# Kernel optimization log

Measured on AMD Instinct MI355X. Metric: run time of the kernel, lower is better.

Reference implementation:

```python
import jax, jax.numpy as jnp
import numpy as np

KH, KW = 3, 3
PAD = 1
C_IN, C_OUT = 64, 128


def unfold(x, kh, kw, pad):
    # x: (B, C, H, W) -> (B, C, kh*kw, H*W), torch.nn.functional.unfold ordering
    B, C, H, W = x.shape
    xp = jnp.pad(x, ((0, 0), (0, 0), (pad, pad), (pad, pad)))
    patches = jnp.stack(
        [xp[:, :, i:i + H, j:j + W] for i in range(kh) for j in range(kw)],
        axis=2,
    )  # (B, C, K, H, W)
    return patches.reshape(B, C, kh * kw, H * W)


def setup_inputs() -> dict:
    key = jax.random.key(0)
    k1, k2, k3 = jax.random.split(key, 3)
    B, H, W = 8, 128, 128
    inp = jax.random.normal(k1, (B, C_IN, H, W), dtype=jnp.float32)
    g_buffer = jax.random.uniform(k2, (B, 2, H, W), dtype=jnp.float32)
    # weights param as in torch: (1, C*kh*kw, 1, out_channels), kaiming-uniform-ish
    wdepth = C_IN * KH * KW
    bound = float(np.sqrt(6.0 / wdepth))
    weights = jax.random.uniform(k3, (1, wdepth, 1, C_OUT), dtype=jnp.float32,
                                 minval=-bound, maxval=bound)
    bias = jnp.zeros((C_OUT,), dtype=jnp.float32)
    return {"input": inp, "g_buffer": g_buffer, "weights": weights, "bias": bias}


def reference(input, g_buffer, weights, bias):
    B, C, H, W = input.shape
    K = KH * KW
    L = H * W
    depth = 2.0 * (g_buffer[:, -1:, :, :] - 0.5)  # (B, 1, H, W)

    input_unf = unfold(input, KH, KW, PAD)          # (B, C, K, L)
    depth_unf = unfold(depth, KH, KW, PAD)          # (B, 1, K, L)

    # bilateral depth weighting
    dfeat = depth_unf - depth.reshape(B, 1, 1, L)   # (B, 1, K, L)
    dfeat = jnp.sum(dfeat * dfeat, axis=1)          # (B, K, L)
    wf = jnp.exp(-dfeat)
    wf = 9.0 * wf / jnp.sum(wf, axis=1, keepdims=True)  # (B, K, L)

    filt = input_unf * wf[:, None, :, :]            # (B, C, K, L)
    filt = filt.reshape(B, C * K, L)

    W2 = weights.reshape(C_OUT, C * K)              # raw reshape, matches torch .view
    out_unf = jnp.einsum('bkl,ok->bol', filt, W2)   # (B, C_OUT, L)
    out = out_unf.reshape(B, C_OUT, H, W) + bias[None, :, None, None]
    return out
```

## Files before the change

kernel.cpp:

```cpp
#include <hip/hip_runtime.h>
#include <hip/hip_bf16.h>
#include <stdint.h>

typedef _Float16 f16x8 __attribute__((ext_vector_type(8)));
typedef float    f32x4 __attribute__((ext_vector_type(4)));

#define CIN   64
#define COUT  128
#define HH    128
#define WW    128
#define BB    8

#define TROW  130
#define ROWBYTES (130 * 128)
#define TSIZE ((size_t)BB * TROW * ROWBYTES)

#define LROWB (34 * 128)
#define NCHKT (4 * 272)

#define AS1 __attribute__((address_space(1)))
#define AS3 __attribute__((address_space(3)))


__global__ void prep_plus(const float* __restrict__ wflat, _Float16* __restrict__ bp,
                          _Float16* __restrict__ T) {
    int gid = blockIdx.x * 256 + threadIdx.x;
    if (gid < 8 * 18 * 64 * 8) {
        int j = gid & 7;
        int l = (gid >> 3) & 63;
        int s = (gid >> 9) % 18;
        int n = gid / (18 * 512);
        int o = n * 16 + (l & 15);
        int c = ((s & 1) << 5) + ((l >> 4) << 3) + j;
        int k = s >> 1;
        bp[gid] = (_Float16)wflat[o * 576 + c * 9 + k];
        return;
    }
    int h = gid - 8 * 18 * 64 * 8;
    if (h < 16 * 1040) {
        int row = h / 1040, c = h - row * 1040;
        int b = row >> 1, yp = (row & 1) * 129;
        f16x8 z = {};
        *(f16x8*)((char*)T + (size_t)(b * TROW + yp) * ROWBYTES + c * 16) = z;
    }
}

__global__ __launch_bounds__(256) void transpose_pass(const float* __restrict__ inp,
                                                      _Float16* __restrict__ T) {
    __shared__ float sT[64][129];
    const int b   = blockIdx.x >> 7;
    const int y   = blockIdx.x & 127;
    const int tid = threadIdx.x;

    const float* ib = inp + ((long)b * CIN * HH + y) * WW;
    const int xq = tid & 31, c8 = tid >> 5;
    #pragma unroll
    for (int i = 0; i < 8; ++i) {
        int c = c8 * 8 + i;
        float4 v = *(const float4*)(ib + (long)c * (HH * WW) + (xq << 2));
        *(float4*)&sT[c][xq << 2] = v;
    }
    __syncthreads();

    const int x  = tid & 127;
    const int ch = tid >> 7;
    char* rowp = (char*)T + (size_t)(b * TROW + y + 1) * ROWBYTES + (size_t)(x + 1) * 128;
    const int sw = (x + 1) & 7;
    for (int c0 = ch * 8; c0 < 64; c0 += 16) {
        f16x8 v;
        #pragma unroll
        for (int j = 0; j < 8; ++j) v[j] = (_Float16)sT[c0 + j][x];
        *(f16x8*)(rowp + (((c0 >> 3) ^ sw) << 4)) = v;
    }
    if (tid < 16) {
        char* basep = (char*)T + (size_t)(b * TROW + y + 1) * ROWBYTES
                    + ((tid >> 3) ? 129 * 128 : 0) + (tid & 7) * 16;
        f16x8 z = {};
        *(f16x8*)basep = z;
    }
}

__global__ __launch_bounds__(256, 4) void depthcnn_main(
    const _Float16* __restrict__ T, const float* __restrict__ gbuf,
    const float* __restrict__ bias, const _Float16* __restrict__ aprep,
    float* __restrict__ out)
{
    __shared__ __align__(1024) char sIn[4 * LROWB];
    __shared__ _Float16 sWf[2][9][36];

    const int blk    = blockIdx.x;
    const int b      = blk & 7;
    const int rest   = blk >> 3;
    const int strip  = rest & 63;
    const int xq     = rest >> 6;
    const int ystart = strip << 1;
    const int x0     = xq << 5;

    const int tid  = threadIdx.x;
    const int wave = tid >> 6;
    const int lane = tid & 63;
    const int oi   = wave;
    const int l15  = lane & 15;
    const int g4   = lane >> 4;

    {
        const char* Tb = (const char*)T + ((size_t)b * TROW + ystart) * ROWBYTES
                       + (size_t)x0 * 128;
        #pragma unroll
        for (int tt = 0; tt < 5; ++tt) {
            int t = tt * 256 + tid;
            if (t < NCHKT) {
                int tr = t / 272, c = t - tr * 272;
                __builtin_amdgcn_global_load_lds(
                    (const AS1 uint32_t*)(Tb + (size_t)tr * ROWBYTES + c * 16),
                    (AS3 uint32_t*)(sIn + tr * LROWB + c * 16), 16, 0, 0);
            }
        }
    }

    const f16x8* __restrict__ ap = (const f16x8*)aprep;
    const char* wp0 = (const char*)ap + (size_t)((oi * 2 + 0) * 18) * 1024 + lane * 16;
    const char* wp1 = (const char*)ap + (size_t)((oi * 2 + 1) * 18) * 1024 + lane * 16;
    f16x8 af[2][2][2];
    af[0][0][0] = *(const f16x8*)(wp0);
    af[0][0][1] = *(const f16x8*)(wp0 + 1024);
    af[0][1][0] = *(const f16x8*)(wp1);
    af[0][1][1] = *(const f16x8*)(wp1 + 1024);

    if (tid < 64) {
        const int r = tid >> 5, pxl = tid & 31, x = x0 + pxl, y = ystart + r;
        const float* g = gbuf + ((size_t)b * 2 + 1) * (HH * WW);
        float dc = 2.f * (g[y * WW + x] - 0.5f);
        float e[9];
        float ssum = 0.f;
        #pragma unroll
        for (int k = 0; k < 9; ++k) {
            int yy = y + (k / 3) - 1;
            int xx = x + (k % 3) - 1;
            float dn = 0.f;
            if ((unsigned)yy < 128u && (unsigned)xx < 128u)
                dn = 2.f * (g[yy * WW + xx] - 0.5f);
            float df = dn - dc;
            float ek = __expf(-df * df);
            e[k] = ek;
            ssum += ek;
        }
        float sc = 9.f / ssum;
        #pragma unroll
        for (int k = 0; k < 9; ++k) sWf[r][k][pxl] = (_Float16)(e[k] * sc);
    }

    __syncthreads();

    const char* binA[3][2];
    #pragma unroll
    for (int d = 0; d < 3; ++d)
        #pragma unroll
        for (int ch = 0; ch < 2; ++ch)
            binA[d][ch] = sIn + (((l15 + d) << 7)
                        + ((((ch << 2) | g4) ^ ((l15 + d) & 7)) << 4));
    const char* bwf = (const char*)&sWf[0][0][0] + l15 * 2;

    f32x4 acc[2][2][2];
    #pragma unroll
    for (int r = 0; r < 2; ++r)
        #pragma unroll
        for (int t2 = 0; t2 < 2; ++t2)
            #pragma unroll
            for (int pt = 0; pt < 2; ++pt)
                acc[r][t2][pt] = (f32x4){0.f, 0.f, 0.f, 0.f};

    #pragma unroll
    for (int k = 0; k < 9; ++k) {
        if (k < 8) {
            const char* q0 = wp0 + (k + 1) * 2048;
            const char* q1 = wp1 + (k + 1) * 2048;
            af[(k + 1) & 1][0][0] = *(const f16x8*)(q0);
            af[(k + 1) & 1][0][1] = *(const f16x8*)(q0 + 1024);
            af[(k + 1) & 1][1][0] = *(const f16x8*)(q1);
            af[(k + 1) & 1][1][1] = *(const f16x8*)(q1 + 1024);
        }
        const int dy = k / 3;
        const int dx = k - 3 * dy;
        #pragma unroll
        for (int r = 0; r < 2; ++r) {
            _Float16 wh[2];
            #pragma unroll
            for (int pt = 0; pt < 2; ++pt)
                wh[pt] = *(const _Float16*)(bwf + ((r * 9 + k) * 72 + pt * 32));
            #pragma unroll
            for (int ch = 0; ch < 2; ++ch) {
                f16x8 bf[2];
                #pragma unroll
                for (int pt = 0; pt < 2; ++pt) {
                    f16x8 iv = *(const f16x8*)(binA[dx][ch]
                             + ((r + dy) * LROWB + (pt << 11)));
                    f16x8 w8 = {wh[pt], wh[pt], wh[pt], wh[pt],
                                wh[pt], wh[pt], wh[pt], wh[pt]};
                    bf[pt] = iv * w8;
                }
                #pragma unroll
                for (int t2 = 0; t2 < 2; ++t2)
                    #pragma unroll
                    for (int pt = 0; pt < 2; ++pt)
                        acc[r][t2][pt] = __builtin_amdgcn_mfma_f32_16x16x32_f16(
                            af[k & 1][t2][ch], bf[pt], acc[r][t2][pt], 0, 0, 0);
            }
        }
    }

    float* ob = out + (size_t)b * COUT * (HH * WW) + x0;
    #pragma unroll
    for (int r = 0; r < 2; ++r) {
        const int y = ystart + r;
        #pragma unroll
        for (int t2 = 0; t2 < 2; ++t2) {
            #pragma unroll
            for (int pt = 0; pt < 2; ++pt) {
                #pragma unroll
                for (int r4 = 0; r4 < 4; ++r4) {
                    const int o = (oi << 5) + (t2 << 4) + (g4 << 2) + r4;
                    ob[(size_t)o * (HH * WW) + (size_t)y * WW + (pt << 4) + l15]
                        = acc[r][t2][pt][r4] + bias[o];
                }
            }
        }
    }
}

extern "C" void kernel_launch(void* const* d_in, const int* in_sizes, int n_in,
                              void* d_out, int out_size, void* d_ws, size_t ws_size,
                              hipStream_t stream) {
    const float* inp  = (const float*)d_in[0];
    const float* gbuf = (const float*)d_in[1];
    const float* wts  = (const float*)d_in[2];
    const float* bias = (const float*)d_in[3];

    _Float16* T  = (_Float16*)d_ws;
    _Float16* bp = (_Float16*)((char*)d_ws + TSIZE);

    hipLaunchKernelGGL(prep_plus, dim3(353), dim3(256), 0, stream, wts, bp, T);
    hipLaunchKernelGGL(transpose_pass, dim3(BB * HH), dim3(256), 0, stream, inp, T);
    hipLaunchKernelGGL(depthcnn_main, dim3(2048), dim3(256), 0, stream,
                       T, gbuf, bias, bp, (float*)d_out);
}
```

Baseline: 49.60 us.

## Process four rows per block with overlapped second-strip halo load

Each block now handles four output rows as two 2-row strips instead of one strip, halving the grid to 1024 blocks. The extra two halo rows and their depth weights are loaded while the first strip's MFMA work runs, so the input halo rows are reused across strips and the load latency is hidden. This trades lower grid parallelism and more LDS per block for less redundant halo traffic and fewer block launches. Weight fragments are reloaded per strip.

```diff
diff --git a/kernel.cpp b/kernel.cpp
--- a/kernel.cpp
+++ b/kernel.cpp
@@ -16,7 +16,6 @@
 #define TSIZE ((size_t)BB * TROW * ROWBYTES)
 
 #define LROWB (34 * 128)
-#define NCHKT (4 * 272)
 
 #define AS1 __attribute__((address_space(1)))
 #define AS3 __attribute__((address_space(3)))
@@ -85,15 +84,15 @@
     const float* __restrict__ bias, const _Float16* __restrict__ aprep,
     float* __restrict__ out)
 {
-    __shared__ __align__(1024) char sIn[4 * LROWB];
-    __shared__ _Float16 sWf[2][9][36];
+    __shared__ __align__(1024) char sIn[6 * LROWB];
+    __shared__ _Float16 sWf[4][9][36];
 
     const int blk    = blockIdx.x;
     const int b      = blk & 7;
     const int rest   = blk >> 3;
-    const int strip  = rest & 63;
-    const int xq     = rest >> 6;
-    const int ystart = strip << 1;
+    const int grp    = rest & 31;
+    const int xq     = rest >> 5;
+    const int ystart = grp << 2;
     const int x0     = xq << 5;
 
     const int tid  = threadIdx.x;
@@ -103,33 +102,28 @@
     const int l15  = lane & 15;
     const int g4   = lane >> 4;
 
-    {
-        const char* Tb = (const char*)T + ((size_t)b * TROW + ystart) * ROWBYTES
-                       + (size_t)x0 * 128;
-        #pragma unroll
-        for (int tt = 0; tt < 5; ++tt) {
-            int t = tt * 256 + tid;
-            if (t < NCHKT) {
-                int tr = t / 272, c = t - tr * 272;
-                __builtin_amdgcn_global_load_lds(
-                    (const AS1 uint32_t*)(Tb + (size_t)tr * ROWBYTES + c * 16),
-                    (AS3 uint32_t*)(sIn + tr * LROWB + c * 16), 16, 0, 0);
-            }
+    const char* Tb = (const char*)T + ((size_t)b * TROW + ystart) * ROWBYTES
+                   + (size_t)x0 * 128;
+    const float* g = gbuf + ((size_t)b * 2 + 1) * (HH * WW);
+
+    #pragma unroll
+    for (int tt = 0; tt < 5; ++tt) {
+        int t = tt * 256 + tid;
+        if (t < 1088) {
+            int tr = t / 272, c = t - tr * 272;
+            __builtin_amdgcn_global_load_lds(
+                (const AS1 uint32_t*)(Tb + (size_t)tr * ROWBYTES + c * 16),
+                (AS3 uint32_t*)(sIn + tr * LROWB + c * 16), 16, 0, 0);
         }
     }
 
     const f16x8* __restrict__ ap = (const f16x8*)aprep;
     const char* wp0 = (const char*)ap + (size_t)((oi * 2 + 0) * 18) * 1024 + lane * 16;
     const char* wp1 = (const char*)ap + (size_t)((oi * 2 + 1) * 18) * 1024 + lane * 16;
-    f16x8 af[2][2][2];
-    af[0][0][0] = *(const f16x8*)(wp0);
-    af[0][0][1] = *(const f16x8*)(wp0 + 1024);
-    af[0][1][0] = *(const f16x8*)(wp1);
-    af[0][1][1] = *(const f16x8*)(wp1 + 1024);
-
-    if (tid < 64) {
-        const int r = tid >> 5, pxl = tid & 31, x = x0 + pxl, y = ystart + r;
-        const float* g = gbuf + ((size_t)b * 2 + 1) * (HH * WW);
+
+    if ((tid & 3) == 0) {
+        const int idx = tid >> 2;
+        const int r = idx >> 5, pxl = idx & 31, x = x0 + pxl, y = ystart + r;
         float dc = 2.f * (g[y * WW + x] - 0.5f);
         float e[9];
         float ssum = 0.f;
@@ -152,6 +146,39 @@
 
     __syncthreads();
 
+    #pragma unroll
+    for (int tt = 0; tt < 3; ++tt) {
+        int t = tt * 256 + tid;
+        if (t < 544) {
+            int tr = t / 272, c = t - tr * 272;
+            __builtin_amdgcn_global_load_lds(
+                (const AS1 uint32_t*)(Tb + (size_t)(4 + tr) * ROWBYTES + c * 16),
+                (AS3 uint32_t*)(sIn + (4 + tr) * LROWB + c * 16), 16, 0, 0);
+        }
+    }
+    if ((tid & 3) == 0) {
+        const int idx = tid >> 2;
+        const int r = 2 + (idx >> 5), pxl = idx & 31, x = x0 + pxl, y = ystart + r;
+        float dc = 2.f * (g[y * WW + x] - 0.5f);
+        float e[9];
+        float ssum = 0.f;
+        #pragma unroll
+        for (int k = 0; k < 9; ++k) {
+            int yy = y + (k / 3) - 1;
+            int xx = x + (k % 3) - 1;
+            float dn = 0.f;
+            if ((unsigned)yy < 128u && (unsigned)xx < 128u)
+                dn = 2.f * (g[yy * WW + xx] - 0.5f);
+            float df = dn - dc;
+            float ek = __expf(-df * df);
+            e[k] = ek;
+            ssum += ek;
+        }
+        float sc = 9.f / ssum;
+        #pragma unroll
+        for (int k = 0; k < 9; ++k) sWf[r][k][pxl] = (_Float16)(e[k] * sc);
+    }
+
     const char* binA[3][2];
     #pragma unroll
     for (int d = 0; d < 3; ++d)
@@ -161,71 +188,86 @@
                         + ((((ch << 2) | g4) ^ ((l15 + d) & 7)) << 4));
     const char* bwf = (const char*)&sWf[0][0][0] + l15 * 2;
 
-    f32x4 acc[2][2][2];
-    #pragma unroll
-    for (int r = 0; r < 2; ++r)
-        #pragma unroll
-        for (int t2 = 0; t2 < 2; ++t2)
-            #pragma unroll
-            for (int pt = 0; pt < 2; ++pt)
-                acc[r][t2][pt] = (f32x4){0.f, 0.f, 0.f, 0.f};
-
-    #pragma unroll
-    for (int k = 0; k < 9; ++k) {
-        if (k < 8) {
-            const char* q0 = wp0 + (k + 1) * 2048;
-            const char* q1 = wp1 + (k + 1) * 2048;
-            af[(k + 1) & 1][0][0] = *(const f16x8*)(q0);
-            af[(k + 1) & 1][0][1] = *(const f16x8*)(q0 + 1024);
-            af[(k + 1) & 1][1][0] = *(const f16x8*)(q1);
-            af[(k + 1) & 1][1][1] = *(const f16x8*)(q1 + 1024);
-        }
-        const int dy = k / 3;
-        const int dx = k - 3 * dy;
-        #pragma unroll
-        for (int r = 0; r < 2; ++r) {
-            _Float16 wh[2];
-            #pragma unroll
-            for (int pt = 0; pt < 2; ++pt)
-                wh[pt] = *(const _Float16*)(bwf + ((r * 9 + k) * 72 + pt * 32));
-            #pragma unroll
-            for (int ch = 0; ch < 2; ++ch) {
-                f16x8 bf[2];
-                #pragma unroll
-                for (int pt = 0; pt < 2; ++pt) {
-                    f16x8 iv = *(const f16x8*)(binA[dx][ch]
-                             + ((r + dy) * LROWB + (pt << 11)));
-                    f16x8 w8 = {wh[pt], wh[pt], wh[pt], wh[pt],
-                                wh[pt], wh[pt], wh[pt], wh[pt]};
-                    bf[pt] = iv * w8;
-                }
-                #pragma unroll
-                for (int t2 = 0; t2 < 2; ++t2)
-                    #pragma unroll
-                    for (int pt = 0; pt < 2; ++pt)
-                        acc[r][t2][pt] = __builtin_amdgcn_mfma_f32_16x16x32_f16(
-                            af[k & 1][t2][ch], bf[pt], acc[r][t2][pt], 0, 0, 0);
-            }
-        }
-    }
-
     float* ob = out + (size_t)b * COUT * (HH * WW) + x0;
-    #pragma unroll
-    for (int r = 0; r < 2; ++r) {
-        const int y = ystart + r;
-        #pragma unroll
-        for (int t2 = 0; t2 < 2; ++t2) {
-            #pragma unroll
-            for (int pt = 0; pt < 2; ++pt) {
-                #pragma unroll
-                for (int r4 = 0; r4 < 4; ++r4) {
-                    const int o = (oi << 5) + (t2 << 4) + (g4 << 2) + r4;
-                    ob[(size_t)o * (HH * WW) + (size_t)y * WW + (pt << 4) + l15]
-                        = acc[r][t2][pt][r4] + bias[o];
-                }
-            }
-        }
-    }
+
+#define KSTRIP(S)                                                                  \
+    {                                                                              \
+        f32x4 acc[2][2][2];                                                        \
+        _Pragma("unroll")                                                          \
+        for (int r = 0; r < 2; ++r)                                                \
+            _Pragma("unroll")                                                      \
+            for (int t2 = 0; t2 < 2; ++t2)                                         \
+                _Pragma("unroll")                                                  \
+                for (int pt = 0; pt < 2; ++pt)                                     \
+                    acc[r][t2][pt] = (f32x4){0.f, 0.f, 0.f, 0.f};                  \
+        f16x8 af[2][2][2];                                                         \
+        af[0][0][0] = *(const f16x8*)(wp0);                                        \
+        af[0][0][1] = *(const f16x8*)(wp0 + 1024);                                 \
+        af[0][1][0] = *(const f16x8*)(wp1);                                        \
+        af[0][1][1] = *(const f16x8*)(wp1 + 1024);                                 \
+        _Pragma("unroll")                                                          \
+        for (int k = 0; k < 9; ++k) {                                              \
+            if (k < 8) {                                                           \
+                const char* q0 = wp0 + (k + 1) * 2048;                             \
+                const char* q1 = wp1 + (k + 1) * 2048;                             \
+                af[(k + 1) & 1][0][0] = *(const f16x8*)(q0);                       \
+                af[(k + 1) & 1][0][1] = *(const f16x8*)(q0 + 1024);                \
+                af[(k + 1) & 1][1][0] = *(const f16x8*)(q1);                       \
+                af[(k + 1) & 1][1][1] = *(const f16x8*)(q1 + 1024);                \
+            }                                                                      \
+            const int dy = k / 3;                                                  \
+            const int dx = k - 3 * dy;                                             \
+            _Pragma("unroll")                                                      \
+            for (int r = 0; r < 2; ++r) {                                          \
+                _Float16 wh[2];                                                    \
+                _Pragma("unroll")                                                  \
+                for (int pt = 0; pt < 2; ++pt)                                     \
+                    wh[pt] = *(const _Float16*)(bwf                                \
+                           + (((2 * (S) + r) * 9 + k) * 72 + pt * 32));            \
+                _Pragma("unroll")                                                  \
+                for (int ch = 0; ch < 2; ++ch) {                                   \
+                    f16x8 bf[2];                                                   \
+                    _Pragma("unroll")                                              \
+                    for (int pt = 0; pt < 2; ++pt) {                               \
+                        f16x8 iv = *(const f16x8*)(binA[dx][ch]                    \
+                                 + ((2 * (S) + r + dy) * LROWB + (pt << 11)));     \
+                        f16x8 w8 = {wh[pt], wh[pt], wh[pt], wh[pt],                \
+                                    wh[pt], wh[pt], wh[pt], wh[pt]};               \
+                        bf[pt] = iv * w8;                                          \
+                    }                                                              \
+                    _Pragma("unroll")                                              \
+                    for (int t2 = 0; t2 < 2; ++t2)                                 \
+                        _Pragma("unroll")                                          \
+                        for (int pt = 0; pt < 2; ++pt)                             \
+                            acc[r][t2][pt] = __builtin_amdgcn_mfma_f32_16x16x32_f16( \
+                                af[k & 1][t2][ch], bf[pt], acc[r][t2][pt], 0, 0, 0); \
+                }                                                                  \
+            }                                                                      \
+        }                                                                          \
+        _Pragma("unroll")                                                          \
+        for (int r = 0; r < 2; ++r) {                                              \
+            const int y = ystart + 2 * (S) + r;                                    \
+            _Pragma("unroll")                                                      \
+            for (int t2 = 0; t2 < 2; ++t2) {                                       \
+                _Pragma("unroll")                                                  \
+                for (int pt = 0; pt < 2; ++pt) {                                   \
+                    _Pragma("unroll")                                              \
+                    for (int r4 = 0; r4 < 4; ++r4) {                               \
+                        const int o = (oi << 5) + (t2 << 4) + (g4 << 2) + r4;      \
+                        ob[(size_t)o * (HH * WW) + (size_t)y * WW + (pt << 4) + l15] \
+                            = acc[r][t2][pt][r4] + bias[o];                        \
+                    }                                                              \
+                }                                                                  \
+            }                                                                      \
+        }                                                                          \
+    }
+
+    KSTRIP(0)
+
+    __syncthreads();
+
+    KSTRIP(1)
+#undef KSTRIP
 }
 
 extern "C" void kernel_launch(void* const* d_in, const int* in_sizes, int n_in,
@@ -241,6 +283,6 @@
 
     hipLaunchKernelGGL(prep_plus, dim3(353), dim3(256), 0, stream, wts, bp, T);
     hipLaunchKernelGGL(transpose_pass, dim3(BB * HH), dim3(256), 0, stream, inp, T);
-    hipLaunchKernelGGL(depthcnn_main, dim3(2048), dim3(256), 0, stream,
+    hipLaunchKernelGGL(depthcnn_main, dim3(1024), dim3(256), 0, stream,
                        T, gbuf, bias, bp, (float*)d_out);
 }
```

New measurement: 58.11 us. 17.2% more time.

## Read activation tiles directly from global memory instead of staging in LDS

Applied to the files above, without the earlier changes.

The main kernel no longer copies the 4-row input halo tile into shared memory with global_load_lds. Each lane now loads its B-operand vectors straight from the transposed fp16 buffer, relying on L1/L2 caching for the 3x3 neighbourhood reuse. The XOR swizzle in the transpose pass is removed to match the plain addressing. This cuts LDS use (raising possible occupancy) and removes the staging step, but puts repeated, partly redundant global loads on the MFMA inner loop's critical path.

```diff
diff --git a/kernel.cpp b/kernel.cpp
--- a/kernel.cpp
+++ b/kernel.cpp
@@ -14,12 +14,6 @@
 #define TROW  130
 #define ROWBYTES (130 * 128)
 #define TSIZE ((size_t)BB * TROW * ROWBYTES)
-
-#define LROWB (34 * 128)
-#define NCHKT (4 * 272)
-
-#define AS1 __attribute__((address_space(1)))
-#define AS3 __attribute__((address_space(3)))
 
 
 __global__ void prep_plus(const float* __restrict__ wflat, _Float16* __restrict__ bp,
@@ -65,12 +59,11 @@
     const int x  = tid & 127;
     const int ch = tid >> 7;
     char* rowp = (char*)T + (size_t)(b * TROW + y + 1) * ROWBYTES + (size_t)(x + 1) * 128;
-    const int sw = (x + 1) & 7;
     for (int c0 = ch * 8; c0 < 64; c0 += 16) {
         f16x8 v;
         #pragma unroll
         for (int j = 0; j < 8; ++j) v[j] = (_Float16)sT[c0 + j][x];
-        *(f16x8*)(rowp + (((c0 >> 3) ^ sw) << 4)) = v;
+        *(f16x8*)(rowp + c0 * 2) = v;
     }
     if (tid < 16) {
         char* basep = (char*)T + (size_t)(b * TROW + y + 1) * ROWBYTES
@@ -85,7 +78,6 @@
     const float* __restrict__ bias, const _Float16* __restrict__ aprep,
     float* __restrict__ out)
 {
-    __shared__ __align__(1024) char sIn[4 * LROWB];
     __shared__ _Float16 sWf[2][9][36];
 
     const int blk    = blockIdx.x;
@@ -103,20 +95,11 @@
     const int l15  = lane & 15;
     const int g4   = lane >> 4;
 
-    {
-        const char* Tb = (const char*)T + ((size_t)b * TROW + ystart) * ROWBYTES
-                       + (size_t)x0 * 128;
-        #pragma unroll
-        for (int tt = 0; tt < 5; ++tt) {
-            int t = tt * 256 + tid;
-            if (t < NCHKT) {
-                int tr = t / 272, c = t - tr * 272;
-                __builtin_amdgcn_global_load_lds(
-                    (const AS1 uint32_t*)(Tb + (size_t)tr * ROWBYTES + c * 16),
-                    (AS3 uint32_t*)(sIn + tr * LROWB + c * 16), 16, 0, 0);
-            }
-        }
-    }
+    const char* Tb = (const char*)T + ((size_t)b * TROW + ystart) * ROWBYTES
+                   + (size_t)x0 * 128 + (l15 << 7) + (g4 << 4);
+    const char* btr[4];
+    #pragma unroll
+    for (int tr = 0; tr < 4; ++tr) btr[tr] = Tb + tr * ROWBYTES;
 
     const f16x8* __restrict__ ap = (const f16x8*)aprep;
     const char* wp0 = (const char*)ap + (size_t)((oi * 2 + 0) * 18) * 1024 + lane * 16;
@@ -152,13 +135,6 @@
 
     __syncthreads();
 
-    const char* binA[3][2];
-    #pragma unroll
-    for (int d = 0; d < 3; ++d)
-        #pragma unroll
-        for (int ch = 0; ch < 2; ++ch)
-            binA[d][ch] = sIn + (((l15 + d) << 7)
-                        + ((((ch << 2) | g4) ^ ((l15 + d) & 7)) << 4));
     const char* bwf = (const char*)&sWf[0][0][0] + l15 * 2;
 
     f32x4 acc[2][2][2];
@@ -193,8 +169,8 @@
                 f16x8 bf[2];
                 #pragma unroll
                 for (int pt = 0; pt < 2; ++pt) {
-                    f16x8 iv = *(const f16x8*)(binA[dx][ch]
-                             + ((r + dy) * LROWB + (pt << 11)));
+                    f16x8 iv = *(const f16x8*)(btr[r + dy]
+                             + ((pt << 11) + dx * 128 + ch * 64));
                     f16x8 w8 = {wh[pt], wh[pt], wh[pt], wh[pt],
                                 wh[pt], wh[pt], wh[pt], wh[pt]};
                     bf[pt] = iv * w8;
```

Result: slower. 83.30 us (+67.9%).

## Retile main kernel so each block covers full row width and all outputs

Applied to the files above, without the earlier changes.

The main conv kernel now assigns each block two full image rows (128 pixels) and has every wave compute all 128 output channels for its own 32-pixel slice, instead of splitting output channels across waves over a 32-pixel window. The block loads whole padded rows into LDS once, which removes the overlapping halo loads and the redundant depth-weight computation done by the previous four x-quarter blocks. Each wave now keeps a larger accumulator set and streams all weight fragments, and MFMA sections are wrapped in s_setprio. The trade-off is a grid that shrinks from 2048 to 512 blocks, more registers and LDS per block, and lower occupancy (launch bounds lowered to 2).

```diff
diff --git a/kernel.cpp b/kernel.cpp
--- a/kernel.cpp
+++ b/kernel.cpp
@@ -14,9 +14,6 @@
 #define TROW  130
 #define ROWBYTES (130 * 128)
 #define TSIZE ((size_t)BB * TROW * ROWBYTES)
-
-#define LROWB (34 * 128)
-#define NCHKT (4 * 272)
 
 #define AS1 __attribute__((address_space(1)))
 #define AS3 __attribute__((address_space(3)))
@@ -80,63 +77,56 @@
     }
 }
 
-__global__ __launch_bounds__(256, 4) void depthcnn_main(
+__global__ __launch_bounds__(256, 2) void depthcnn_main(
     const _Float16* __restrict__ T, const float* __restrict__ gbuf,
     const float* __restrict__ bias, const _Float16* __restrict__ aprep,
     float* __restrict__ out)
 {
-    __shared__ __align__(1024) char sIn[4 * LROWB];
-    __shared__ _Float16 sWf[2][9][36];
+    __shared__ __align__(1024) char sIn[4 * ROWBYTES];
+    __shared__ _Float16 sWf[2][9][128];
 
     const int blk    = blockIdx.x;
     const int b      = blk & 7;
-    const int rest   = blk >> 3;
-    const int strip  = rest & 63;
-    const int xq     = rest >> 6;
+    const int strip  = blk >> 3;
     const int ystart = strip << 1;
-    const int x0     = xq << 5;
 
     const int tid  = threadIdx.x;
     const int wave = tid >> 6;
     const int lane = tid & 63;
-    const int oi   = wave;
     const int l15  = lane & 15;
     const int g4   = lane >> 4;
+    const int x0w  = wave << 5;
 
     {
-        const char* Tb = (const char*)T + ((size_t)b * TROW + ystart) * ROWBYTES
-                       + (size_t)x0 * 128;
-        #pragma unroll
-        for (int tt = 0; tt < 5; ++tt) {
+        const char* Tb = (const char*)T + ((size_t)b * TROW + ystart) * ROWBYTES;
+        #pragma unroll
+        for (int tt = 0; tt < 17; ++tt) {
             int t = tt * 256 + tid;
-            if (t < NCHKT) {
-                int tr = t / 272, c = t - tr * 272;
+            if (t < 4 * 1040) {
+                int tr = t / 1040, c = t - tr * 1040;
                 __builtin_amdgcn_global_load_lds(
                     (const AS1 uint32_t*)(Tb + (size_t)tr * ROWBYTES + c * 16),
-                    (AS3 uint32_t*)(sIn + tr * LROWB + c * 16), 16, 0, 0);
-            }
-        }
-    }
-
-    const f16x8* __restrict__ ap = (const f16x8*)aprep;
-    const char* wp0 = (const char*)ap + (size_t)((oi * 2 + 0) * 18) * 1024 + lane * 16;
-    const char* wp1 = (const char*)ap + (size_t)((oi * 2 + 1) * 18) * 1024 + lane * 16;
-    f16x8 af[2][2][2];
-    af[0][0][0] = *(const f16x8*)(wp0);
-    af[0][0][1] = *(const f16x8*)(wp0 + 1024);
-    af[0][1][0] = *(const f16x8*)(wp1);
-    af[0][1][1] = *(const f16x8*)(wp1 + 1024);
-
-    if (tid < 64) {
-        const int r = tid >> 5, pxl = tid & 31, x = x0 + pxl, y = ystart + r;
+                    (AS3 uint32_t*)(sIn + tr * ROWBYTES + c * 16), 16, 0, 0);
+            }
+        }
+    }
+
+    const char* ap = (const char*)aprep + lane * 16;
+    f16x8 af[2][8];
+    #pragma unroll
+    for (int ot = 0; ot < 8; ++ot)
+        af[0][ot] = *(const f16x8*)(ap + (size_t)(ot * 18) * 1024);
+
+    {
+        const int r = tid >> 7, px = tid & 127, y = ystart + r;
         const float* g = gbuf + ((size_t)b * 2 + 1) * (HH * WW);
-        float dc = 2.f * (g[y * WW + x] - 0.5f);
+        float dc = 2.f * (g[y * WW + px] - 0.5f);
         float e[9];
         float ssum = 0.f;
         #pragma unroll
         for (int k = 0; k < 9; ++k) {
             int yy = y + (k / 3) - 1;
-            int xx = x + (k % 3) - 1;
+            int xx = px + (k % 3) - 1;
             float dn = 0.f;
             if ((unsigned)yy < 128u && (unsigned)xx < 128u)
                 dn = 2.f * (g[yy * WW + xx] - 0.5f);
@@ -147,7 +137,7 @@
         }
         float sc = 9.f / ssum;
         #pragma unroll
-        for (int k = 0; k < 9; ++k) sWf[r][k][pxl] = (_Float16)(e[k] * sc);
+        for (int k = 0; k < 9; ++k) sWf[r][k][px] = (_Float16)(e[k] * sc);
     }
 
     __syncthreads();
@@ -157,71 +147,71 @@
     for (int d = 0; d < 3; ++d)
         #pragma unroll
         for (int ch = 0; ch < 2; ++ch)
-            binA[d][ch] = sIn + (((l15 + d) << 7)
+            binA[d][ch] = sIn + (x0w << 7) + (((l15 + d) << 7)
                         + ((((ch << 2) | g4) ^ ((l15 + d) & 7)) << 4));
-    const char* bwf = (const char*)&sWf[0][0][0] + l15 * 2;
-
-    f32x4 acc[2][2][2];
+    const char* bwf = (const char*)&sWf[0][0][0] + ((x0w + l15) << 1);
+
+    f32x4 acc[2][2][8];
     #pragma unroll
     for (int r = 0; r < 2; ++r)
         #pragma unroll
-        for (int t2 = 0; t2 < 2; ++t2)
-            #pragma unroll
-            for (int pt = 0; pt < 2; ++pt)
-                acc[r][t2][pt] = (f32x4){0.f, 0.f, 0.f, 0.f};
-
-    #pragma unroll
-    for (int k = 0; k < 9; ++k) {
-        if (k < 8) {
-            const char* q0 = wp0 + (k + 1) * 2048;
-            const char* q1 = wp1 + (k + 1) * 2048;
-            af[(k + 1) & 1][0][0] = *(const f16x8*)(q0);
-            af[(k + 1) & 1][0][1] = *(const f16x8*)(q0 + 1024);
-            af[(k + 1) & 1][1][0] = *(const f16x8*)(q1);
-            af[(k + 1) & 1][1][1] = *(const f16x8*)(q1 + 1024);
-        }
-        const int dy = k / 3;
-        const int dx = k - 3 * dy;
+        for (int pt = 0; pt < 2; ++pt)
+            #pragma unroll
+            for (int ot = 0; ot < 8; ++ot)
+                acc[r][pt][ot] = (f32x4){0.f, 0.f, 0.f, 0.f};
+
+    #pragma unroll
+    for (int s = 0; s < 18; ++s) {
+        if (s < 17) {
+            #pragma unroll
+            for (int ot = 0; ot < 8; ++ot)
+                af[(s + 1) & 1][ot] = *(const f16x8*)(ap + (size_t)(ot * 18 + s + 1) * 1024);
+        }
+        const int tap = s >> 1;
+        const int ch  = s & 1;
+        const int dy  = tap / 3;
+        const int dx  = tap - 3 * dy;
         #pragma unroll
         for (int r = 0; r < 2; ++r) {
             _Float16 wh[2];
             #pragma unroll
             for (int pt = 0; pt < 2; ++pt)
-                wh[pt] = *(const _Float16*)(bwf + ((r * 9 + k) * 72 + pt * 32));
-            #pragma unroll
-            for (int ch = 0; ch < 2; ++ch) {
-                f16x8 bf[2];
+                wh[pt] = *(const _Float16*)(bwf + ((r * 9 + tap) * 256 + pt * 32));
+            f16x8 bf[2];
+            #pragma unroll
+            for (int pt = 0; pt < 2; ++pt) {
+                f16x8 iv = *(const f16x8*)(binA[dx][ch]
+                         + ((r + dy) * ROWBYTES + (pt << 11)));
+                f16x8 w8 = {wh[pt], wh[pt], wh[pt], wh[pt],
+                            wh[pt], wh[pt], wh[pt], wh[pt]};
+                bf[pt] = iv * w8;
+            }
+            __builtin_amdgcn_s_setprio(1);
+            #pragma unroll
+            for (int ot = 0; ot < 8; ++ot) {
+                acc[r][0][ot] = __builtin_amdgcn_mfma_f32_16x16x32_f16(
+                    af[s & 1][ot], bf[0], acc[r][0][ot], 0, 0, 0);
+                acc[r][1][ot] = __builtin_amdgcn_mfma_f32_16x16x32_f16(
+                    af[s & 1][ot], bf[1], acc[r][1][ot], 0, 0, 0);
+            }
+            __builtin_amdgcn_s_setprio(0);
+        }
+    }
+
+    float* ob = out + (size_t)b * COUT * (HH * WW);
+    #pragma unroll
+    for (int ot = 0; ot < 8; ++ot) {
+        #pragma unroll
+        for (int r4 = 0; r4 < 4; ++r4) {
+            const int o = (ot << 4) + (g4 << 2) + r4;
+            const float bv = bias[o];
+            #pragma unroll
+            for (int r = 0; r < 2; ++r) {
                 #pragma unroll
                 for (int pt = 0; pt < 2; ++pt) {
-                    f16x8 iv = *(const f16x8*)(binA[dx][ch]
-                             + ((r + dy) * LROWB + (pt << 11)));
-                    f16x8 w8 = {wh[pt], wh[pt], wh[pt], wh[pt],
-                                wh[pt], wh[pt], wh[pt], wh[pt]};
-                    bf[pt] = iv * w8;
-                }
-                #pragma unroll
-                for (int t2 = 0; t2 < 2; ++t2)
-                    #pragma unroll
-                    for (int pt = 0; pt < 2; ++pt)
-                        acc[r][t2][pt] = __builtin_amdgcn_mfma_f32_16x16x32_f16(
-                            af[k & 1][t2][ch], bf[pt], acc[r][t2][pt], 0, 0, 0);
-            }
-        }
-    }
-
-    float* ob = out + (size_t)b * COUT * (HH * WW) + x0;
-    #pragma unroll
-    for (int r = 0; r < 2; ++r) {
-        const int y = ystart + r;
-        #pragma unroll
-        for (int t2 = 0; t2 < 2; ++t2) {
-            #pragma unroll
-            for (int pt = 0; pt < 2; ++pt) {
-                #pragma unroll
-                for (int r4 = 0; r4 < 4; ++r4) {
-                    const int o = (oi << 5) + (t2 << 4) + (g4 << 2) + r4;
-                    ob[(size_t)o * (HH * WW) + (size_t)y * WW + (pt << 4) + l15]
-                        = acc[r][t2][pt][r4] + bias[o];
+                    const int px = x0w + (pt << 4) + l15;
+                    ob[(size_t)o * (HH * WW) + (size_t)(ystart + r) * WW + px]
+                        = acc[r][pt][ot][r4] + bv;
                 }
             }
         }
@@ -241,6 +231,6 @@
 
     hipLaunchKernelGGL(prep_plus, dim3(353), dim3(256), 0, stream, wts, bp, T);
     hipLaunchKernelGGL(transpose_pass, dim3(BB * HH), dim3(256), 0, stream, inp, T);
-    hipLaunchKernelGGL(depthcnn_main, dim3(2048), dim3(256), 0, stream,
+    hipLaunchKernelGGL(depthcnn_main, dim3(512), dim3(256), 0, stream,
                        T, gbuf, bias, bp, (float*)d_out);
 }
```

Result: faster. 47.58 us, median of 4 (-4.1%).
